# Performance work log

Hardware: AMD Instinct MI355X
Metric: run time of the kernel (lower is better)

## Reference

```python
import jax, jax.numpy as jnp
import numpy as np

C = 32          # in/out channels per spnn.Conv3d(32, 32, 2, stride=2)
KVOL = 8        # 2^3 kernel offsets
GRID = 128      # voxel grid resolution
N_RAW = 1_000_000


def setup_inputs() -> dict:
    rng = np.random.default_rng(0)
    # unique active voxel coordinates (torchsparse coords are unique)
    coords = np.unique(rng.integers(0, GRID, size=(N_RAW, 3), dtype=np.int32), axis=0)
    n = coords.shape[0]
    # kernel=2, stride=2: each input voxel hits exactly one output voxel
    out_coords = coords // 2
    k_idx = (coords[:, 0] % 2) * 4 + (coords[:, 1] % 2) * 2 + (coords[:, 2] % 2)
    _, out_idx = np.unique(out_coords, axis=0, return_inverse=True)
    num_out = int(out_idx.max()) + 1

    key = jax.random.key(0)
    kx, kw = jax.random.split(key)
    x = jax.random.normal(kx, (n, C), dtype=jnp.float32)
    W = jax.random.normal(kw, (KVOL, C, C), dtype=jnp.float32) * 0.05
    return {
        "x": x,
        "W": W,
        "k_idx": jnp.asarray(k_idx, dtype=jnp.int32),
        "out_idx": jnp.asarray(out_idx, dtype=jnp.int32),
        "num_out": num_out,
    }


def reference(x, W, k_idx, out_idx, num_out):
    # gather -> per-offset GEMM -> scatter-add (sparse conv kernel-map form)
    # proj[n, k, d] = sum_c x[n, c] * W[k, c, d]
    proj = jnp.einsum("nc,kcd->nkd", x, W)
    # pick the projection for each point's kernel offset: [n, C]
    sel = jnp.take_along_axis(proj, k_idx[:, None, None], axis=1)[:, 0, :]
    # scatter-add into output voxels
    out = jax.ops.segment_sum(sel, out_idx, num_segments=num_out)
    return out
```

## Files before the change

kernel.cpp:

```cpp
#include <hip/hip_runtime.h>
#include <hip/hip_bf16.h>


typedef __attribute__((ext_vector_type(8))) short bf16x8;
typedef __attribute__((ext_vector_type(4))) float f32x4;

union ABFrag { bf16x8 v; int i[4]; };

__device__ __forceinline__ unsigned short f2bf(float f) {
    union { float f; unsigned u; } v; v.f = f;
    unsigned r = v.u + 0x7FFFu + ((v.u >> 16) & 1u);
    return (unsigned short)(r >> 16);
}

__global__ void prep_w_kernel(const float* __restrict__ W,
                              unsigned short* __restrict__ WB) {
    int t = blockIdx.x * blockDim.x + threadIdx.x;
    if (t >= 8 * 2 * 64 * 8) return;
    int j    = t & 7;
    int lane = (t >> 3) & 63;
    int half = (t >> 9) & 1;
    int k    = t >> 10;
    int c = (lane >> 4) * 8 + j;
    int d = half * 16 + (lane & 15);
    WB[t] = f2bf(W[k * 1024 + c * 32 + d]);
}

__global__ __launch_bounds__(256) void conv_kernel(
    const float* __restrict__ x,
    const unsigned short* __restrict__ WB,
    const int* __restrict__ k_idx,
    const int* __restrict__ out_idx,
    float* __restrict__ out,
    int n)
{
    const int lane = threadIdx.x & 63;
    const int wv   = threadIdx.x >> 6;
    const int base = (blockIdx.x * 4 + wv) * 16;
    if (base >= n) return;

    const int row  = lane & 15;
    const int quad = lane >> 4;
    const int p = base + row;

    int krow = -1;
    ABFrag a; a.i[0] = 0; a.i[1] = 0; a.i[2] = 0; a.i[3] = 0;
    if (p < n) {
        krow = k_idx[p];
        const float* xp = x + (size_t)p * 32 + quad * 8;
        float4 x0 = *(const float4*)xp;
        float4 x1 = *(const float4*)(xp + 4);
        unsigned short h0 = f2bf(x0.x), h1 = f2bf(x0.y), h2 = f2bf(x0.z), h3 = f2bf(x0.w);
        unsigned short h4 = f2bf(x1.x), h5 = f2bf(x1.y), h6 = f2bf(x1.z), h7 = f2bf(x1.w);
        a.i[0] = (int)h0 | ((int)h1 << 16);
        a.i[1] = (int)h2 | ((int)h3 << 16);
        a.i[2] = (int)h4 | ((int)h5 << 16);
        a.i[3] = (int)h6 | ((int)h7 << 16);
    }

    f32x4 acc0 = {0.f, 0.f, 0.f, 0.f};
    f32x4 acc1 = {0.f, 0.f, 0.f, 0.f};

#pragma unroll
    for (int k = 0; k < 8; ++k) {
        bf16x8 b0 = *(const bf16x8*)(WB + ((size_t)(k * 2 + 0) * 64 + lane) * 8);
        bf16x8 b1 = *(const bf16x8*)(WB + ((size_t)(k * 2 + 1) * 64 + lane) * 8);
        const bool keep = (krow == k);
        ABFrag ak;
        ak.i[0] = keep ? a.i[0] : 0;
        ak.i[1] = keep ? a.i[1] : 0;
        ak.i[2] = keep ? a.i[2] : 0;
        ak.i[3] = keep ? a.i[3] : 0;
        acc0 = __builtin_amdgcn_mfma_f32_16x16x32_bf16(ak.v, b0, acc0, 0, 0, 0);
        acc1 = __builtin_amdgcn_mfma_f32_16x16x32_bf16(ak.v, b1, acc1, 0, 0, 0);
    }

#pragma unroll
    for (int r = 0; r < 4; ++r) {
        int m = quad * 4 + r;
        int p2 = base + m;
        if (p2 < n) {
            int oi = out_idx[p2];
            float* op = out + (size_t)oi * 32 + (lane & 15);
            atomicAdd(op,      acc0[r]);
            atomicAdd(op + 16, acc1[r]);
        }
    }
}

extern "C" void kernel_launch(void* const* d_in, const int* in_sizes, int n_in,
                              void* d_out, int out_size, void* d_ws, size_t ws_size,
                              hipStream_t stream) {
    const float* x       = (const float*)d_in[0];
    const float* W       = (const float*)d_in[1];
    const int*   k_idx   = (const int*)d_in[2];
    const int*   out_idx = (const int*)d_in[3];
    const int n = in_sizes[2];

    unsigned short* WB = (unsigned short*)d_ws;
    float* out = (float*)d_out;

    hipMemsetAsync(d_out, 0, (size_t)out_size * sizeof(float), stream);

    prep_w_kernel<<<32, 256, 0, stream>>>(W, WB);

    int blocks = (n + 63) / 64;
    if (blocks > 0)
        conv_kernel<<<blocks, 256, 0, stream>>>(x, WB, k_idx, out_idx, out, n);
}
```

Before: 219.2 us.

## Replace atomic scatter with inverted child map and per-output gather GEMM

Builds a dense output-to-child map (num_out x 8 input indices) in workspace, then computes each output voxel by gathering up to eight child rows and accumulating all kernel offsets in MFMA, with plain stores instead of atomics. This removes the output memset and the float atomics, and the MFMA work is no longer masked with zeros. It adds a map memset and a build pass, plus scattered row gathers. An atomic fallback is kept for when the workspace is too small.

```diff
diff --git a/kernel.cpp b/kernel.cpp
--- a/kernel.cpp
+++ b/kernel.cpp
@@ -26,36 +26,46 @@
     WB[t] = f2bf(W[k * 1024 + c * 32 + d]);
 }
 
-__global__ __launch_bounds__(256) void conv_kernel(
+__global__ __launch_bounds__(256) void build_map_kernel(
+    const int* __restrict__ k_idx, const int* __restrict__ out_idx,
+    int* __restrict__ child, int n) {
+    int t = blockIdx.x * blockDim.x + threadIdx.x;
+    if (t < n) child[(size_t)out_idx[t] * 8 + k_idx[t]] = t;
+}
+
+__global__ __launch_bounds__(256) void conv_gather_kernel(
     const float* __restrict__ x,
     const unsigned short* __restrict__ WB,
-    const int* __restrict__ k_idx,
-    const int* __restrict__ out_idx,
+    const int* __restrict__ child,
     float* __restrict__ out,
-    int n)
+    int num_out)
 {
-    const int lane = threadIdx.x & 63;
-    const int wv   = threadIdx.x >> 6;
-    const int base = (blockIdx.x * 4 + wv) * 16;
-    if (base >= n) return;
+    const int lane  = threadIdx.x & 63;
+    const int wv    = threadIdx.x >> 6;
+    const int obase = (blockIdx.x * 4 + wv) * 16;
+    if (obase >= num_out) return;
 
     const int row  = lane & 15;
     const int quad = lane >> 4;
-    const int p = base + row;
+    const int o = obase + row;
 
-    int krow = -1;
-    ABFrag a; a.i[0] = 0; a.i[1] = 0; a.i[2] = 0; a.i[3] = 0;
-    if (p < n) {
-        krow = k_idx[p];
-        const float* xp = x + (size_t)p * 32 + quad * 8;
-        float4 x0 = *(const float4*)xp;
-        float4 x1 = *(const float4*)(xp + 4);
-        unsigned short h0 = f2bf(x0.x), h1 = f2bf(x0.y), h2 = f2bf(x0.z), h3 = f2bf(x0.w);
-        unsigned short h4 = f2bf(x1.x), h5 = f2bf(x1.y), h6 = f2bf(x1.z), h7 = f2bf(x1.w);
-        a.i[0] = (int)h0 | ((int)h1 << 16);
-        a.i[1] = (int)h2 | ((int)h3 << 16);
-        a.i[2] = (int)h4 | ((int)h5 << 16);
-        a.i[3] = (int)h6 | ((int)h7 << 16);
+    int4 c0 = make_int4(-1, -1, -1, -1), c1 = make_int4(-1, -1, -1, -1);
+    if (o < num_out) {
+        const int4* cp = (const int4*)(child + (size_t)o * 8);
+        c0 = cp[0]; c1 = cp[1];
+    }
+    int pk[8] = {c0.x, c0.y, c0.z, c0.w, c1.x, c1.y, c1.z, c1.w};
+
+    float4 xa[8], xb[8];
+#pragma unroll
+    for (int k = 0; k < 8; ++k) {
+        xa[k] = make_float4(0.f, 0.f, 0.f, 0.f);
+        xb[k] = make_float4(0.f, 0.f, 0.f, 0.f);
+        if (pk[k] >= 0) {
+            const float* xp = x + (size_t)pk[k] * 32 + quad * 8;
+            xa[k] = *(const float4*)xp;
+            xb[k] = *(const float4*)(xp + 4);
+        }
     }
 
     f32x4 acc0 = {0.f, 0.f, 0.f, 0.f};
@@ -63,22 +73,66 @@
 
 #pragma unroll
     for (int k = 0; k < 8; ++k) {
+        ABFrag a;
+        a.i[0] = (int)f2bf(xa[k].x) | ((int)f2bf(xa[k].y) << 16);
+        a.i[1] = (int)f2bf(xa[k].z) | ((int)f2bf(xa[k].w) << 16);
+        a.i[2] = (int)f2bf(xb[k].x) | ((int)f2bf(xb[k].y) << 16);
+        a.i[3] = (int)f2bf(xb[k].z) | ((int)f2bf(xb[k].w) << 16);
         bf16x8 b0 = *(const bf16x8*)(WB + ((size_t)(k * 2 + 0) * 64 + lane) * 8);
         bf16x8 b1 = *(const bf16x8*)(WB + ((size_t)(k * 2 + 1) * 64 + lane) * 8);
-        const bool keep = (krow == k);
-        ABFrag ak;
-        ak.i[0] = keep ? a.i[0] : 0;
-        ak.i[1] = keep ? a.i[1] : 0;
-        ak.i[2] = keep ? a.i[2] : 0;
-        ak.i[3] = keep ? a.i[3] : 0;
-        acc0 = __builtin_amdgcn_mfma_f32_16x16x32_bf16(ak.v, b0, acc0, 0, 0, 0);
-        acc1 = __builtin_amdgcn_mfma_f32_16x16x32_bf16(ak.v, b1, acc1, 0, 0, 0);
+        acc0 = __builtin_amdgcn_mfma_f32_16x16x32_bf16(a.v, b0, acc0, 0, 0, 0);
+        acc1 = __builtin_amdgcn_mfma_f32_16x16x32_bf16(a.v, b1, acc1, 0, 0, 0);
     }
 
 #pragma unroll
     for (int r = 0; r < 4; ++r) {
-        int m = quad * 4 + r;
-        int p2 = base + m;
+        int oo = obase + quad * 4 + r;
+        if (oo < num_out) {
+            float* op = out + (size_t)oo * 32 + (lane & 15);
+            op[0]  = acc0[r];
+            op[16] = acc1[r];
+        }
+    }
+}
+
+__global__ __launch_bounds__(256) void conv_atomic_kernel(
+    const float* __restrict__ x, const unsigned short* __restrict__ WB,
+    const int* __restrict__ k_idx, const int* __restrict__ out_idx,
+    float* __restrict__ out, int n)
+{
+    const int lane = threadIdx.x & 63;
+    const int wv   = threadIdx.x >> 6;
+    const int base = (blockIdx.x * 4 + wv) * 16;
+    if (base >= n) return;
+    const int row = lane & 15, quad = lane >> 4;
+    const int p = base + row;
+    int krow = -1;
+    ABFrag a; a.i[0] = a.i[1] = a.i[2] = a.i[3] = 0;
+    if (p < n) {
+        krow = k_idx[p];
+        const float* xp = x + (size_t)p * 32 + quad * 8;
+        float4 x0 = *(const float4*)xp;
+        float4 x1 = *(const float4*)(xp + 4);
+        a.i[0] = (int)f2bf(x0.x) | ((int)f2bf(x0.y) << 16);
+        a.i[1] = (int)f2bf(x0.z) | ((int)f2bf(x0.w) << 16);
+        a.i[2] = (int)f2bf(x1.x) | ((int)f2bf(x1.y) << 16);
+        a.i[3] = (int)f2bf(x1.z) | ((int)f2bf(x1.w) << 16);
+    }
+    f32x4 acc0 = {0.f,0.f,0.f,0.f}, acc1 = {0.f,0.f,0.f,0.f};
+#pragma unroll
+    for (int k = 0; k < 8; ++k) {
+        bf16x8 b0 = *(const bf16x8*)(WB + ((size_t)(k*2+0)*64 + lane)*8);
+        bf16x8 b1 = *(const bf16x8*)(WB + ((size_t)(k*2+1)*64 + lane)*8);
+        const bool keep = (krow == k);
+        ABFrag ak;
+        ak.i[0] = keep ? a.i[0] : 0; ak.i[1] = keep ? a.i[1] : 0;
+        ak.i[2] = keep ? a.i[2] : 0; ak.i[3] = keep ? a.i[3] : 0;
+        acc0 = __builtin_amdgcn_mfma_f32_16x16x32_bf16(ak.v, b0, acc0, 0, 0, 0);
+        acc1 = __builtin_amdgcn_mfma_f32_16x16x32_bf16(ak.v, b1, acc1, 0, 0, 0);
+    }
+#pragma unroll
+    for (int r = 0; r < 4; ++r) {
+        int p2 = base + quad * 4 + r;
         if (p2 < n) {
             int oi = out_idx[p2];
             float* op = out + (size_t)oi * 32 + (lane & 15);
@@ -96,15 +150,24 @@
     const int*   k_idx   = (const int*)d_in[2];
     const int*   out_idx = (const int*)d_in[3];
     const int n = in_sizes[2];
+    const int num_out = out_size / 32;
+    float* out = (float*)d_out;
 
     unsigned short* WB = (unsigned short*)d_ws;
-    float* out = (float*)d_out;
-
-    hipMemsetAsync(d_out, 0, (size_t)out_size * sizeof(float), stream);
+    const size_t wb_bytes = 16384;
+    int* child = (int*)((char*)d_ws + wb_bytes);
+    const size_t child_bytes = (size_t)num_out * 8 * sizeof(int);
 
     prep_w_kernel<<<32, 256, 0, stream>>>(W, WB);
 
-    int blocks = (n + 63) / 64;
-    if (blocks > 0)
-        conv_kernel<<<blocks, 256, 0, stream>>>(x, WB, k_idx, out_idx, out, n);
+    if (ws_size >= wb_bytes + child_bytes) {
+        hipMemsetAsync(child, 0xFF, child_bytes, stream);
+        build_map_kernel<<<(n + 255) / 256, 256, 0, stream>>>(k_idx, out_idx, child, n);
+        int blocks = (num_out + 63) / 64;
+        conv_gather_kernel<<<blocks, 256, 0, stream>>>(x, WB, child, out, num_out);
+    } else {
+        hipMemsetAsync(d_out, 0, (size_t)out_size * sizeof(float), stream);
+        int blocks = (n + 63) / 64;
+        conv_atomic_kernel<<<blocks, 256, 0, stream>>>(x, WB, k_idx, out_idx, out, n);
+    }
 }
```

Result: faster. 181.7 us (-17.1%).
